# Optimization experiments

Measured on AMD Instinct MI355X. Metric: run time of the kernel, lower is better.

The kernel has to match this reference:

```python
import jax, jax.numpy as jnp
import numpy as np

DECAY = 0.9        # membrane leak factor per step (prms['decay'])
V_TH = 1.0         # spike threshold (prms['v_th'])
SUR_SCALE = 4.0    # surrogate-gradient sharpness (prms['surrogate_scale'])


def _spike(v):
    """Heaviside spike in forward; sigmoid surrogate in backward (straight-through)."""
    hard = (v >= V_TH).astype(v.dtype)
    sur = jax.nn.sigmoid(SUR_SCALE * (v - V_TH))
    return sur + jax.lax.stop_gradient(hard - sur)


def setup_inputs() -> dict:
    key = jax.random.key(0)
    k1, k2, k3 = jax.random.split(key, 3)
    B, T, P, D = 64, 256, 1024, 1024
    prv_voltage = jax.random.normal(k1, (B, T, P), dtype=jnp.float32)
    prv_spikes = (jax.random.uniform(k2, (B, T, P)) < 0.1).astype(jnp.float32)
    weights = jax.random.normal(k3, (P, D), dtype=jnp.float32) / np.float32(np.sqrt(P))
    return {"prv_voltage": prv_voltage, "prv_spikes": prv_spikes, "weights": weights}


def reference(prv_voltage, prv_spikes, weights):
    # synaptic currents for every step at once: (B, T, D)
    currents = jnp.einsum('btp,pd->btd', prv_spikes, weights)

    def step(v, i_t):
        v_new = DECAY * v + i_t            # leak + integrate
        s = _spike(v_new)                  # threshold
        v_next = v_new * (1.0 - s)         # reset-to-zero on spike
        return v_next, (v_new, s)

    B, T, D = currents.shape
    v0 = jnp.zeros((B, D), dtype=currents.dtype)
    _, (vs, ss) = jax.lax.scan(step, v0, jnp.swapaxes(currents, 0, 1))  # scan over time
    voltage = jnp.swapaxes(vs, 0, 1)  # (B, T, D)
    spikes = jnp.swapaxes(ss, 0, 1)   # (B, T, D)
    return voltage, spikes
```

## Files before the change

### kernel.cpp

```cpp
#include <hip/hip_runtime.h>


#define LIF_B 64
#define LIF_T 256
#define LIF_P 1024
#define LIF_D 1024
#define LIF_N ((size_t)LIF_B * LIF_T * LIF_D)

__global__ __launch_bounds__(256) void lif_currents_kernel(
    const float* __restrict__ spikes,
    const float* __restrict__ W,
    float* __restrict__ cur_out)
{
    __shared__ unsigned long long smask[16];
    __shared__ int plist[1024];
    __shared__ int scnt[2];

    const int row  = blockIdx.x;
    const int tid  = threadIdx.x;
    const int lane = tid & 63;
    const int wave = tid >> 6;
    const int dbase = wave << 8;

    const float* srow = spikes + (size_t)row * LIF_P;
    const float* wcol = W + dbase + (lane << 2);

    for (int jj = 0; jj < 4; ++jj) {
        const int j = (wave << 2) + jj;
        const float sv = srow[(j << 6) + lane];
        const unsigned long long m = __ballot(sv != 0.0f);
        if (lane == 0) smask[j] = m;
    }
    __syncthreads();

    if (wave == 0) {
        unsigned long long m = (lane < 16) ? smask[lane] : 0ULL;
        const int pc = __popcll(m);
        int s = pc;
        for (int d = 1; d < 8; d <<= 1) {
            const int vps = __shfl_up(s, d, 8);
            if ((lane & 7) >= d) s += vps;
        }
        if (lane == 7)  scnt[0] = s;
        if (lane == 15) scnt[1] = s;
        if (lane < 16) {
            int idx = ((lane < 8) ? 0 : 512) + (s - pc);
            const int pb = lane << 6;
            while (m) {
                plist[idx++] = pb + __builtin_ctzll(m);
                m &= (m - 1);
            }
        }
    }
    __syncthreads();

    const int c0 = scnt[0];
    const int c1 = scnt[1];

    float a0x=0.f,a0y=0.f,a0z=0.f,a0w=0.f;
    float a1x=0.f,a1y=0.f,a1z=0.f,a1w=0.f;

    #define LIF_ACC(AX,AY,AZ,AW,WV)                                             \
        AX = __fadd_rn(AX, (WV).x); AY = __fadd_rn(AY, (WV).y);                  \
        AZ = __fadd_rn(AZ, (WV).z); AW = __fadd_rn(AW, (WV).w);

    #define LIF_PANEL(BASE, CNT, AX,AY,AZ,AW)                                    \
    {                                                                            \
        int i = 0;                                                               \
        for (; i + 4 <= (CNT); i += 4) {                                         \
            const int4 ps = *reinterpret_cast<const int4*>(&plist[(BASE) + i]);  \
            const float4 w0 = *reinterpret_cast<const float4*>(wcol + ((size_t)ps.x << 10)); \
            const float4 w1 = *reinterpret_cast<const float4*>(wcol + ((size_t)ps.y << 10)); \
            const float4 w2 = *reinterpret_cast<const float4*>(wcol + ((size_t)ps.z << 10)); \
            const float4 w3 = *reinterpret_cast<const float4*>(wcol + ((size_t)ps.w << 10)); \
            LIF_ACC(AX,AY,AZ,AW, w0) LIF_ACC(AX,AY,AZ,AW, w1)                    \
            LIF_ACC(AX,AY,AZ,AW, w2) LIF_ACC(AX,AY,AZ,AW, w3)                    \
        }                                                                        \
        for (; i < (CNT); ++i) {                                                 \
            const int p = plist[(BASE) + i];                                     \
            const float4 wv = *reinterpret_cast<const float4*>(wcol + ((size_t)p << 10)); \
            LIF_ACC(AX,AY,AZ,AW, wv)                                             \
        }                                                                        \
    }

    LIF_PANEL(0,   c0, a0x,a0y,a0z,a0w)
    LIF_PANEL(512, c1, a1x,a1y,a1z,a1w)
    #undef LIF_PANEL
    #undef LIF_ACC

    float4 c;
    c.x = __fadd_rn(a0x, a1x);
    c.y = __fadd_rn(a0y, a1y);
    c.z = __fadd_rn(a0z, a1z);
    c.w = __fadd_rn(a0w, a1w);

    *reinterpret_cast<float4*>(cur_out + (size_t)row * LIF_D + dbase + (lane << 2)) = c;
}

__global__ __launch_bounds__(256) void lif_scan_kernel(
    float* __restrict__ voltage,
    float* __restrict__ spikes_out)
{
    const int tid = blockIdx.x * 256 + threadIdx.x;
    const int b = tid >> 10;
    const int d = tid & (LIF_D - 1);

    float v = 0.0f;
    const size_t base = ((size_t)b * LIF_T) * LIF_D + d;

    float p0 = voltage[base + 0*(size_t)LIF_D];
    float p1 = voltage[base + 1*(size_t)LIF_D];
    float p2 = voltage[base + 2*(size_t)LIF_D];
    float p3 = voltage[base + 3*(size_t)LIF_D];

    for (int t = 0; t < LIF_T; t += 4) {
        const float c0 = p0, c1 = p1, c2 = p2, c3 = p3;
        if (t + 4 < LIF_T) {
            p0 = voltage[base + (size_t)(t + 4) * LIF_D];
            p1 = voltage[base + (size_t)(t + 5) * LIF_D];
            p2 = voltage[base + (size_t)(t + 6) * LIF_D];
            p3 = voltage[base + (size_t)(t + 7) * LIF_D];
        }
        const size_t i0 = base + (size_t)t * LIF_D;
        {
            const float vn = __fadd_rn(__fmul_rn(0.9f, v), c0);
            const bool f = (vn >= 1.0f);
            voltage[i0 + 0*(size_t)LIF_D] = vn;
            spikes_out[i0 + 0*(size_t)LIF_D] = f ? 1.0f : 0.0f;
            v = f ? 0.0f : vn;
        }
        {
            const float vn = __fadd_rn(__fmul_rn(0.9f, v), c1);
            const bool f = (vn >= 1.0f);
            voltage[i0 + 1*(size_t)LIF_D] = vn;
            spikes_out[i0 + 1*(size_t)LIF_D] = f ? 1.0f : 0.0f;
            v = f ? 0.0f : vn;
        }
        {
            const float vn = __fadd_rn(__fmul_rn(0.9f, v), c2);
            const bool f = (vn >= 1.0f);
            voltage[i0 + 2*(size_t)LIF_D] = vn;
            spikes_out[i0 + 2*(size_t)LIF_D] = f ? 1.0f : 0.0f;
            v = f ? 0.0f : vn;
        }
        {
            const float vn = __fadd_rn(__fmul_rn(0.9f, v), c3);
            const bool f = (vn >= 1.0f);
            voltage[i0 + 3*(size_t)LIF_D] = vn;
            spikes_out[i0 + 3*(size_t)LIF_D] = f ? 1.0f : 0.0f;
            v = f ? 0.0f : vn;
        }
    }
}

extern "C" void kernel_launch(void* const* d_in, const int* in_sizes, int n_in,
                              void* d_out, int out_size, void* d_ws, size_t ws_size,
                              hipStream_t stream) {
    (void)in_sizes; (void)n_in; (void)out_size; (void)d_ws; (void)ws_size;

    const float* spikes = (const float*)d_in[1];
    const float* W      = (const float*)d_in[2];

    float* out        = (float*)d_out;
    float* voltage    = out;
    float* spikes_out = out + LIF_N;

    lif_currents_kernel<<<LIF_B * LIF_T, 256, 0, stream>>>(spikes, W, voltage);
    lif_scan_kernel<<<(LIF_B * LIF_D) / 256, 256, 0, stream>>>(voltage, spikes_out);
}
```

Measured before the change: 272.1 us.

## Tile sparse spike matmul over 32 rows with LDS-staged weight panels

The currents kernel now gives each block 32 time rows and one quarter of D. It stages 64x256 weight panels into LDS with direct global-to-LDS loads, so each weight row is fetched once per block instead of once per spike-row gather. Spike bitmasks for all 32 rows are built up front, and each wave accumulates its 8 rows from LDS using the mask bits. This trades scattered global gathers for dense streaming of all of W per block, which costs 16 barrier-synchronised stages without double buffering. It also raises register and LDS use, which limits occupancy.

```diff
diff --git a/kernel.cpp b/kernel.cpp
--- a/kernel.cpp
+++ b/kernel.cpp
@@ -12,89 +12,113 @@
     const float* __restrict__ W,
     float* __restrict__ cur_out)
 {
-    __shared__ unsigned long long smask[16];
-    __shared__ int plist[1024];
-    __shared__ int scnt[2];
+    __shared__ float4 wbuf[64 * 64];
+    __shared__ unsigned long long masks[32][16];
 
-    const int row  = blockIdx.x;
     const int tid  = threadIdx.x;
     const int lane = tid & 63;
     const int wave = tid >> 6;
-    const int dbase = wave << 8;
+    const int bid  = blockIdx.x;
+    const int ds   = bid >> 9;
+    const int rg   = bid & 511;
+    const int row0 = rg << 5;
+    const int dbase = ds << 8;
 
-    const float* srow = spikes + (size_t)row * LIF_P;
-    const float* wcol = W + dbase + (lane << 2);
-
-    for (int jj = 0; jj < 4; ++jj) {
-        const int j = (wave << 2) + jj;
-        const float sv = srow[(j << 6) + lane];
-        const unsigned long long m = __ballot(sv != 0.0f);
-        if (lane == 0) smask[j] = m;
-    }
-    __syncthreads();
-
-    if (wave == 0) {
-        unsigned long long m = (lane < 16) ? smask[lane] : 0ULL;
-        const int pc = __popcll(m);
-        int s = pc;
-        for (int d = 1; d < 8; d <<= 1) {
-            const int vps = __shfl_up(s, d, 8);
-            if ((lane & 7) >= d) s += vps;
-        }
-        if (lane == 7)  scnt[0] = s;
-        if (lane == 15) scnt[1] = s;
-        if (lane < 16) {
-            int idx = ((lane < 8) ? 0 : 512) + (s - pc);
-            const int pb = lane << 6;
-            while (m) {
-                plist[idx++] = pb + __builtin_ctzll(m);
-                m &= (m - 1);
-            }
+    for (int i = 0; i < 8; ++i) {
+        const int rl = (wave << 3) + i;
+        const float* srow = spikes + (size_t)(row0 + rl) * LIF_P;
+        #pragma unroll 4
+        for (int c = 0; c < 16; ++c) {
+            const float sv = srow[(c << 6) + lane];
+            const unsigned long long m = __ballot(sv != 0.0f);
+            if (lane == 0) masks[rl][c] = m;
         }
     }
-    __syncthreads();
 
-    const int c0 = scnt[0];
-    const int c1 = scnt[1];
-
-    float a0x=0.f,a0y=0.f,a0z=0.f,a0w=0.f;
-    float a1x=0.f,a1y=0.f,a1z=0.f,a1w=0.f;
-
-    #define LIF_ACC(AX,AY,AZ,AW,WV)                                             \
-        AX = __fadd_rn(AX, (WV).x); AY = __fadd_rn(AY, (WV).y);                  \
-        AZ = __fadd_rn(AZ, (WV).z); AW = __fadd_rn(AW, (WV).w);
-
-    #define LIF_PANEL(BASE, CNT, AX,AY,AZ,AW)                                    \
-    {                                                                            \
-        int i = 0;                                                               \
-        for (; i + 4 <= (CNT); i += 4) {                                         \
-            const int4 ps = *reinterpret_cast<const int4*>(&plist[(BASE) + i]);  \
-            const float4 w0 = *reinterpret_cast<const float4*>(wcol + ((size_t)ps.x << 10)); \
-            const float4 w1 = *reinterpret_cast<const float4*>(wcol + ((size_t)ps.y << 10)); \
-            const float4 w2 = *reinterpret_cast<const float4*>(wcol + ((size_t)ps.z << 10)); \
-            const float4 w3 = *reinterpret_cast<const float4*>(wcol + ((size_t)ps.w << 10)); \
-            LIF_ACC(AX,AY,AZ,AW, w0) LIF_ACC(AX,AY,AZ,AW, w1)                    \
-            LIF_ACC(AX,AY,AZ,AW, w2) LIF_ACC(AX,AY,AZ,AW, w3)                    \
-        }                                                                        \
-        for (; i < (CNT); ++i) {                                                 \
-            const int p = plist[(BASE) + i];                                     \
-            const float4 wv = *reinterpret_cast<const float4*>(wcol + ((size_t)p << 10)); \
-            LIF_ACC(AX,AY,AZ,AW, wv)                                             \
-        }                                                                        \
+    float4 accA[8], accB[8];
+    #pragma unroll
+    for (int i = 0; i < 8; ++i) {
+        accA[i] = make_float4(0.f, 0.f, 0.f, 0.f);
+        accB[i] = make_float4(0.f, 0.f, 0.f, 0.f);
     }
 
-    LIF_PANEL(0,   c0, a0x,a0y,a0z,a0w)
-    LIF_PANEL(512, c1, a1x,a1y,a1z,a1w)
-    #undef LIF_PANEL
-    #undef LIF_ACC
+    #define LIF_ACC4(A, WV)                                                   \
+        (A).x = __fadd_rn((A).x, (WV).x); (A).y = __fadd_rn((A).y, (WV).y);   \
+        (A).z = __fadd_rn((A).z, (WV).z); (A).w = __fadd_rn((A).w, (WV).w);
 
-    float4 c;
-    c.x = __fadd_rn(a0x, a1x);
-    c.y = __fadd_rn(a0y, a1y);
-    c.z = __fadd_rn(a0z, a1z);
-    c.w = __fadd_rn(a0w, a1w);
+    #define LIF_STAGE(C)                                                      \
+    {                                                                         \
+        const float* gsrc = W + ((size_t)(((C) << 6) + (wave << 4)) << 10)    \
+                              + dbase + (lane << 2);                          \
+        char* lbase = (char*)wbuf + ((wave << 4) << 10);                      \
+        _Pragma("unroll")                                                     \
+        for (int i = 0; i < 16; ++i) {                                        \
+            __builtin_amdgcn_global_load_lds(                                 \
+                (const __attribute__((address_space(1))) void*)(gsrc + ((size_t)i << 10)), \
+                (__attribute__((address_space(3))) void*)(lbase + (i << 10)), \
+                16, 0, 0);                                                    \
+        }                                                                     \
+    }
 
-    *reinterpret_cast<float4*>(cur_out + (size_t)row * LIF_D + dbase + (lane << 2)) = c;
+    #define LIF_COMPUTE(C, ACC)                                               \
+    {                                                                         \
+        _Pragma("unroll")                                                     \
+        for (int i = 0; i < 8; ++i) {                                         \
+            unsigned long long m = masks[(wave << 3) + i][(C)];               \
+            m = ((unsigned long long)__builtin_amdgcn_readfirstlane(          \
+                     (unsigned)(m >> 32)) << 32)                              \
+              | (unsigned)__builtin_amdgcn_readfirstlane((unsigned)m);        \
+            while (m) {                                                       \
+                const int p0 = __builtin_ctzll(m); m &= (m - 1);              \
+                const float4 w0 = wbuf[(p0 << 6) | lane];                     \
+                if (m) {                                                      \
+                    const int p1 = __builtin_ctzll(m); m &= (m - 1);          \
+                    const float4 w1 = wbuf[(p1 << 6) | lane];                 \
+                    if (m) {                                                  \
+                        const int p2 = __builtin_ctzll(m); m &= (m - 1);      \
+                        const float4 w2 = wbuf[(p2 << 6) | lane];             \
+                        if (m) {                                              \
+                            const int p3 = __builtin_ctzll(m); m &= (m - 1);  \
+                            const float4 w3 = wbuf[(p3 << 6) | lane];         \
+                            LIF_ACC4(ACC[i], w0) LIF_ACC4(ACC[i], w1)         \
+                            LIF_ACC4(ACC[i], w2) LIF_ACC4(ACC[i], w3)         \
+                        } else {                                              \
+                            LIF_ACC4(ACC[i], w0) LIF_ACC4(ACC[i], w1)         \
+                            LIF_ACC4(ACC[i], w2)                              \
+                        }                                                     \
+                    } else { LIF_ACC4(ACC[i], w0) LIF_ACC4(ACC[i], w1) }      \
+                } else { LIF_ACC4(ACC[i], w0) }                               \
+            }                                                                 \
+        }                                                                     \
+    }
+
+    #define LIF_CHUNK(C, ACC)                                                 \
+        __syncthreads();                                                      \
+        LIF_STAGE(C)                                                          \
+        asm volatile("s_waitcnt vmcnt(0)" ::: "memory");                      \
+        __syncthreads();                                                      \
+        LIF_COMPUTE(C, ACC)
+
+    LIF_CHUNK(0,  accA) LIF_CHUNK(1,  accA) LIF_CHUNK(2,  accA) LIF_CHUNK(3,  accA)
+    LIF_CHUNK(4,  accA) LIF_CHUNK(5,  accA) LIF_CHUNK(6,  accA) LIF_CHUNK(7,  accA)
+    LIF_CHUNK(8,  accB) LIF_CHUNK(9,  accB) LIF_CHUNK(10, accB) LIF_CHUNK(11, accB)
+    LIF_CHUNK(12, accB) LIF_CHUNK(13, accB) LIF_CHUNK(14, accB) LIF_CHUNK(15, accB)
+
+    #undef LIF_CHUNK
+    #undef LIF_COMPUTE
+    #undef LIF_STAGE
+    #undef LIF_ACC4
+
+    #pragma unroll
+    for (int i = 0; i < 8; ++i) {
+        float4 c4;
+        c4.x = __fadd_rn(accA[i].x, accB[i].x);
+        c4.y = __fadd_rn(accA[i].y, accB[i].y);
+        c4.z = __fadd_rn(accA[i].z, accB[i].z);
+        c4.w = __fadd_rn(accA[i].w, accB[i].w);
+        const int row = row0 + (wave << 3) + i;
+        *reinterpret_cast<float4*>(cur_out + (size_t)row * LIF_D + dbase + (lane << 2)) = c4;
+    }
 }
 
 __global__ __launch_bounds__(256) void lif_scan_kernel(
@@ -108,10 +132,10 @@
     float v = 0.0f;
     const size_t base = ((size_t)b * LIF_T) * LIF_D + d;
 
-    float p0 = voltage[base + 0*(size_t)LIF_D];
-    float p1 = voltage[base + 1*(size_t)LIF_D];
-    float p2 = voltage[base + 2*(size_t)LIF_D];
-    float p3 = voltage[base + 3*(size_t)LIF_D];
+    float p0 = voltage[base + 0 * (size_t)LIF_D];
+    float p1 = voltage[base + 1 * (size_t)LIF_D];
+    float p2 = voltage[base + 2 * (size_t)LIF_D];
+    float p3 = voltage[base + 3 * (size_t)LIF_D];
 
     for (int t = 0; t < LIF_T; t += 4) {
         const float c0 = p0, c1 = p1, c2 = p2, c3 = p3;
@@ -125,29 +149,29 @@
         {
             const float vn = __fadd_rn(__fmul_rn(0.9f, v), c0);
             const bool f = (vn >= 1.0f);
-            voltage[i0 + 0*(size_t)LIF_D] = vn;
-            spikes_out[i0 + 0*(size_t)LIF_D] = f ? 1.0f : 0.0f;
+            voltage[i0 + 0 * (size_t)LIF_D] = vn;
+            spikes_out[i0 + 0 * (size_t)LIF_D] = f ? 1.0f : 0.0f;
             v = f ? 0.0f : vn;
         }
         {
             const float vn = __fadd_rn(__fmul_rn(0.9f, v), c1);
             const bool f = (vn >= 1.0f);
-            voltage[i0 + 1*(size_t)LIF_D] = vn;
-            spikes_out[i0 + 1*(size_t)LIF_D] = f ? 1.0f : 0.0f;
+            voltage[i0 + 1 * (size_t)LIF_D] = vn;
+            spikes_out[i0 + 1 * (size_t)LIF_D] = f ? 1.0f : 0.0f;
             v = f ? 0.0f : vn;
         }
         {
             const float vn = __fadd_rn(__fmul_rn(0.9f, v), c2);
             const bool f = (vn >= 1.0f);
-            voltage[i0 + 2*(size_t)LIF_D] = vn;
-            spikes_out[i0 + 2*(size_t)LIF_D] = f ? 1.0f : 0.0f;
+            voltage[i0 + 2 * (size_t)LIF_D] = vn;
+            spikes_out[i0 + 2 * (size_t)LIF_D] = f ? 1.0f : 0.0f;
             v = f ? 0.0f : vn;
         }
         {
             const float vn = __fadd_rn(__fmul_rn(0.9f, v), c3);
             const bool f = (vn >= 1.0f);
-            voltage[i0 + 3*(size_t)LIF_D] = vn;
-            spikes_out[i0 + 3*(size_t)LIF_D] = f ? 1.0f : 0.0f;
+            voltage[i0 + 3 * (size_t)LIF_D] = vn;
+            spikes_out[i0 + 3 * (size_t)LIF_D] = f ? 1.0f : 0.0f;
             v = f ? 0.0f : vn;
         }
     }
@@ -165,6 +189,6 @@
     float* voltage    = out;
     float* spikes_out = out + LIF_N;
 
-    lif_currents_kernel<<<LIF_B * LIF_T, 256, 0, stream>>>(spikes, W, voltage);
+    lif_currents_kernel<<<2048, 256, 0, stream>>>(spikes, W, voltage);
     lif_scan_kernel<<<(LIF_B * LIF_D) / 256, 256, 0, stream>>>(voltage, spikes_out);
 }
```

New measurement: 414.2 us. 52.2% more time.
